# Performance work log

Measured on AMD Instinct MI355X. Metric: run time of the kernel, lower is better.

## Reference

```python
import jax, jax.numpy as jnp
import numpy as np

B, S, E, H, D = 384, 128, 512, 4, 128  # batch, seq(block), embed, heads, head_dim


def setup_inputs() -> dict:
    key = jax.random.key(0)
    ks = jax.random.split(key, 6)
    scale = 1.0 / np.sqrt(E)  # lecun_normal-ish fan-in scaling
    return {
        "x": jax.random.normal(ks[0], (B, S, E), dtype=jnp.float32),
        "Wq": jax.random.normal(ks[1], (E, E), dtype=jnp.float32) * scale,
        "bq": jnp.zeros((E,), dtype=jnp.float32),
        "Wk": jax.random.normal(ks[2], (E, E), dtype=jnp.float32) * scale,
        "bk": jnp.zeros((E,), dtype=jnp.float32),
        "Wv": jax.random.normal(ks[3], (E, E), dtype=jnp.float32) * scale,
        "bv": jnp.zeros((E,), dtype=jnp.float32),
        "Wo": jax.random.normal(ks[4], (E, E), dtype=jnp.float32) * scale,
        "bo": jnp.zeros((E,), dtype=jnp.float32),
    }


def reference(x, Wq, bq, Wk, bk, Wv, bv, Wo, bo):
    # Projections, then split heads: [B,S,E] -> [B,S,H,D]
    q = (x @ Wq + bq).reshape(B, S, H, D)
    k = (x @ Wk + bk).reshape(B, S, H, D)
    v = (x @ Wv + bv).reshape(B, S, H, D)
    # NOTE: original applies no 1/sqrt(D) scaling and no mask.
    scores = jnp.einsum("BSHD,BTHD->BHST", q, k)  # [B,H,S,T]
    weights = jax.nn.softmax(scores, axis=-1)
    out = jnp.einsum("BHST,BTHD->BSHD", weights, v).reshape(B, S, E)
    return out @ Wo + bo
```

## Files before the change

kernel.cpp:

```cpp
#include <hip/hip_runtime.h>
#include <hip/hip_bf16.h>
#include <cstdint>


#define EMB 512

typedef __attribute__((ext_vector_type(4))) float    f32x4;
typedef __attribute__((ext_vector_type(8))) _Float16 f16x8;

#define MFMA16(a, b, c) __builtin_amdgcn_mfma_f32_16x16x32_f16((a), (b), (c), 0, 0, 0)

__device__ __forceinline__ int swz128(int row, int col) {
    return row * 128 + (col ^ (((row >> 2) & 3) << 4));
}
__device__ __forceinline__ int swz64(int row, int col) {
    return row * 64 + (col ^ (((row >> 2) & 3) << 4));
}

__device__ __forceinline__ void gld_lds16(const _Float16* g, _Float16* l) {
    __builtin_amdgcn_global_load_lds(
        (const __attribute__((address_space(1))) void*)g,
        (__attribute__((address_space(3))) void*)l, 16, 0, 0);
}

__device__ __forceinline__ void stage64(_Float16* lds, const _Float16* gbase,
                                        int grow0, int k0, int wave, int lane) {
#pragma unroll
    for (int i = 0; i < 4; ++i) {
        int idx = wave * 256 + i * 64 + lane;
        int n   = idx >> 3;
        int kb  = (idx & 7) ^ (((n >> 2) & 3) << 1);
        gld_lds16(gbase + (grow0 + n) * EMB + k0 + kb * 8,
                  lds + wave * 2048 + i * 512);
    }
}

#define ZACC(A)                                   \
    _Pragma("unroll") for (int _i = 0; _i < 2; ++_i) \
    _Pragma("unroll") for (int _j = 0; _j < 8; ++_j) \
        A[_i][_j] = (f32x4){0.f, 0.f, 0.f, 0.f};

__global__ void k_prep(const float* __restrict__ x, _Float16* __restrict__ xh,
                       const float* __restrict__ Wq, const float* __restrict__ Wk,
                       const float* __restrict__ Wv, const float* __restrict__ Wo,
                       _Float16* __restrict__ Wqkvt, _Float16* __restrict__ Wot) {
    __shared__ float t[32][33];
    const int g = blockIdx.x, tid = threadIdx.x;
    if (g < 12288) {
        long i = ((long)g * 256 + tid) * 8;
        f32x4 a = *(const f32x4*)(x + i);
        f32x4 b = *(const f32x4*)(x + i + 4);
        f16x8 o;
        o[0] = (_Float16)a[0]; o[1] = (_Float16)a[1];
        o[2] = (_Float16)a[2]; o[3] = (_Float16)a[3];
        o[4] = (_Float16)b[0]; o[5] = (_Float16)b[1];
        o[6] = (_Float16)b[2]; o[7] = (_Float16)b[3];
        *(f16x8*)(xh + i) = o;
        return;
    }
    const int tb = g - 12288;
    const int z = tb >> 8, t2 = tb & 255;
    const float* W = (z == 0) ? Wq : (z == 1) ? Wk : (z == 2) ? Wv : Wo;
    _Float16* Wt = (z < 3) ? (Wqkvt + (long)z * 512 * EMB) : Wot;
    const int tx = tid & 31, ty = tid >> 5;
    const int k0 = (t2 & 15) * 32, n0 = (t2 >> 4) * 32;
#pragma unroll
    for (int i = 0; i < 4; ++i)
        t[ty + i * 8][tx] = W[(k0 + ty + i * 8) * EMB + n0 + tx];
    __syncthreads();
#pragma unroll
    for (int i = 0; i < 4; ++i)
        Wt[(n0 + ty + i * 8) * EMB + k0 + tx] = (_Float16)t[tx][ty + i * 8];
}

__global__ __launch_bounds__(256, 4)
void k_qkv(const _Float16* __restrict__ xh, const _Float16* __restrict__ Wqkvt,
           const float* __restrict__ bq, const float* __restrict__ bk,
           const float* __restrict__ bv,
           _Float16* __restrict__ qb, _Float16* __restrict__ kb,
           _Float16* __restrict__ vtb) {
    __shared__ _Float16 S[2][128 * 64];
    _Float16* SA = S[0];
    _Float16* SB = S[1];
    const int tid = threadIdx.x, wave = tid >> 6, lane = tid & 63;
    const int l15 = lane & 15, quad = lane >> 4;
    const int g = blockIdx.x;
    const int xcd = g & 7, r = g >> 3;
    const int bb = xcd * 48 + r / 12, j = r % 12;
    const int m0 = bb * 128;
    const bool vswap = (j >= 8);
    const _Float16* As = vswap ? SB : SA;
    const _Float16* Bs = vswap ? SA : SB;
    f32x4 acc[2][8];
    ZACC(acc);
    for (int k0 = 0; k0 < EMB; k0 += 64) {
        stage64(SA, xh, m0, k0, wave, lane);
        stage64(SB, Wqkvt, j * 128, k0, wave, lane);
        __syncthreads();
#pragma unroll
        for (int ktl = 0; ktl < 2; ++ktl) {
            int cb = ktl * 32 + quad * 8;
            f16x8 a0 = *(const f16x8*)&As[swz64(wave * 32 + l15, cb)];
            f16x8 a1 = *(const f16x8*)&As[swz64(wave * 32 + 16 + l15, cb)];
#pragma unroll
            for (int nt = 0; nt < 8; ++nt) {
                f16x8 bbf = *(const f16x8*)&Bs[swz64(nt * 16 + l15, cb)];
                acc[0][nt] = MFMA16(a0, bbf, acc[0][nt]);
                acc[1][nt] = MFMA16(a1, bbf, acc[1][nt]);
            }
        }
        __syncthreads();
    }
    _Float16* SC = &S[0][0];
    if (!vswap) {
        const float* bias = (j < 4) ? bq : bk;
        const int nc0 = (j & 3) * 128;
#pragma unroll
        for (int nt = 0; nt < 8; ++nt) {
            int col = nt * 16 + l15;
            float bz = bias[nc0 + col];
#pragma unroll
            for (int mt = 0; mt < 2; ++mt)
#pragma unroll
                for (int rr = 0; rr < 4; ++rr) {
                    int row = wave * 32 + mt * 16 + quad * 4 + rr;
                    SC[swz128(row, col)] = (_Float16)(acc[mt][nt][rr] + bz);
                }
        }
        __syncthreads();
        _Float16* dst = (j < 4) ? qb : kb;
#pragma unroll
        for (int i = 0; i < 8; ++i) {
            int idx = i * 256 + tid;
            int row = idx >> 4, col = (idx & 15) * 8;
            f16x8 v = *(const f16x8*)&SC[row * 128 + (col ^ (((row >> 2) & 3) << 4))];
            *(f16x8*)(dst + (long)(m0 + row) * EMB + nc0 + col) = v;
        }
    } else {
        const int hv = j - 8;
#pragma unroll
        for (int mt = 0; mt < 2; ++mt)
#pragma unroll
            for (int rr = 0; rr < 4; ++rr) {
                int row = wave * 32 + mt * 16 + quad * 4 + rr;
                float bz = bv[hv * 128 + row];
#pragma unroll
                for (int nt = 0; nt < 8; ++nt) {
                    int col = nt * 16 + l15;
                    SC[swz128(row, col)] = (_Float16)(acc[mt][nt][rr] + bz);
                }
            }
        __syncthreads();
        _Float16* dst = vtb + (long)(bb * 4 + hv) * 128 * 128;
#pragma unroll
        for (int i = 0; i < 8; ++i) {
            int idx = i * 256 + tid;
            int row = idx >> 4, col = (idx & 15) * 8;
            f16x8 v = *(const f16x8*)&SC[row * 128 + (col ^ (((row >> 2) & 3) << 4))];
            *(f16x8*)(dst + row * 128 + col) = v;
        }
    }
}

__global__ __launch_bounds__(512, 4)
void k_core(const _Float16* __restrict__ qb, const _Float16* __restrict__ kb,
            const _Float16* __restrict__ vtb, _Float16* __restrict__ attn) {
    __shared__ _Float16 SK[128 * 128];
    __shared__ _Float16 SV[128 * 128];
    const int tid = threadIdx.x, wave = tid >> 6, lane = tid & 63;
    const int l15 = lane & 15, quad = lane >> 4;
    const int g = blockIdx.x;
    const int xcd = g & 7, r = g >> 3;
    const int b = xcd * 48 + (r >> 2), h = r & 3;
    const int sRow0 = b * 128, wRow0 = h * 128;
    const _Float16* vt = vtb + (long)(b * 4 + h) * 128 * 128;

    f16x8 qf[4];
#pragma unroll
    for (int kt = 0; kt < 4; ++kt)
        qf[kt] = *(const f16x8*)(qb + (long)(sRow0 + wave * 16 + l15) * EMB +
                                 wRow0 + kt * 32 + quad * 8);
    __builtin_amdgcn_sched_barrier(0);
#pragma unroll
    for (int i = 0; i < 4; ++i) {
        int seg = i * 8 + wave;
        int idx = seg * 64 + lane;
        int n   = idx >> 4;
        int kbk = (idx & 15) ^ (((n >> 2) & 3) << 1);
        gld_lds16(kb + (long)(sRow0 + n) * EMB + wRow0 + kbk * 8, SK + seg * 512);
    }
    __builtin_amdgcn_sched_barrier(0);
#pragma unroll
    for (int i = 0; i < 4; ++i) {
        int seg = i * 8 + wave;
        int idx = seg * 64 + lane;
        int n   = idx >> 4;
        int kbk = (idx & 15) ^ (((n >> 2) & 3) << 1);
        gld_lds16(vt + n * 128 + kbk * 8, SV + seg * 512);
    }
    asm volatile("s_waitcnt vmcnt(4)" ::: "memory");
    __builtin_amdgcn_sched_barrier(0);
    __builtin_amdgcn_s_barrier();

    f32x4 acc[8];
#pragma unroll
    for (int nt = 0; nt < 8; ++nt) acc[nt] = (f32x4){0.f, 0.f, 0.f, 0.f};

    __builtin_amdgcn_s_setprio(1);
#pragma unroll
    for (int kt = 0; kt < 4; ++kt) {
        int ca = kt * 32 + quad * 8;
#pragma unroll
        for (int nt = 0; nt < 8; ++nt) {
            f16x8 kf = *(const f16x8*)&SK[swz128(nt * 16 + l15, ca)];
            acc[nt] = MFMA16(qf[kt], kf, acc[nt]);
        }
    }
    __builtin_amdgcn_s_setprio(0);
#pragma unroll
    for (int rr = 0; rr < 4; ++rr) {
        float mx = acc[0][rr];
#pragma unroll
        for (int nt = 1; nt < 8; ++nt) mx = fmaxf(mx, acc[nt][rr]);
        mx = fmaxf(mx, __shfl_xor(mx, 1));
        mx = fmaxf(mx, __shfl_xor(mx, 2));
        mx = fmaxf(mx, __shfl_xor(mx, 4));
        mx = fmaxf(mx, __shfl_xor(mx, 8));
        float sm = 0.f;
#pragma unroll
        for (int nt = 0; nt < 8; ++nt) {
            float e = __expf(acc[nt][rr] - mx);
            acc[nt][rr] = e;
            sm += e;
        }
        sm += __shfl_xor(sm, 1);
        sm += __shfl_xor(sm, 2);
        sm += __shfl_xor(sm, 4);
        sm += __shfl_xor(sm, 8);
        float inv = 1.0f / sm;
#pragma unroll
        for (int nt = 0; nt < 8; ++nt) acc[nt][rr] *= inv;
    }
    __syncthreads();

#pragma unroll
    for (int nt = 0; nt < 8; ++nt) {
        int col = nt * 16 + l15;
#pragma unroll
        for (int rr = 0; rr < 4; ++rr)
            SK[swz128(wave * 16 + quad * 4 + rr, col)] = (_Float16)acc[nt][rr];
    }
    __syncthreads();

#pragma unroll
    for (int nt = 0; nt < 8; ++nt) acc[nt] = (f32x4){0.f, 0.f, 0.f, 0.f};
    __builtin_amdgcn_s_setprio(1);
#pragma unroll
    for (int kt = 0; kt < 4; ++kt) {
        int ca = kt * 32 + quad * 8;
        f16x8 p0 = *(const f16x8*)&SK[swz128(wave * 16 + l15, ca)];
#pragma unroll
        for (int nt = 0; nt < 8; ++nt) {
            f16x8 vf = *(const f16x8*)&SV[swz128(nt * 16 + l15, ca)];
            acc[nt] = MFMA16(p0, vf, acc[nt]);
        }
    }
    __builtin_amdgcn_s_setprio(0);
    __syncthreads();

#pragma unroll
    for (int nt = 0; nt < 8; ++nt) {
        int col = nt * 16 + l15;
#pragma unroll
        for (int rr = 0; rr < 4; ++rr)
            SV[swz128(wave * 16 + quad * 4 + rr, col)] = (_Float16)acc[nt][rr];
    }
    __syncthreads();
#pragma unroll
    for (int i = 0; i < 4; ++i) {
        int idx = i * 512 + tid;
        int row = idx >> 4, col = (idx & 15) * 8;
        f16x8 v = *(const f16x8*)&SV[row * 128 + (col ^ (((row >> 2) & 3) << 4))];
        *(f16x8*)(attn + (long)(sRow0 + row) * EMB + wRow0 + col) = v;
    }
}

__global__ __launch_bounds__(256, 4)
void k_out(const _Float16* __restrict__ attn, const _Float16* __restrict__ Wot,
           const float* __restrict__ bo, float* __restrict__ out) {
    __shared__ _Float16 SH[16384];
    _Float16* SA = SH;
    _Float16* SB = SH + 4096;
    const int tid = threadIdx.x, wave = tid >> 6, lane = tid & 63;
    const int l15 = lane & 15, quad = lane >> 4;
    const int g = blockIdx.x;
    const int xcd = g & 7, r = g >> 3;
    const int m0 = (xcd * 96 + (r >> 2)) * 64, n0 = (r & 3) * 128;
    f32x4 acc[8];
#pragma unroll
    for (int nt = 0; nt < 8; ++nt) acc[nt] = (f32x4){0.f, 0.f, 0.f, 0.f};
    for (int k0 = 0; k0 < EMB; k0 += 64) {
#pragma unroll
        for (int i = 0; i < 2; ++i) {
            int seg = i * 4 + wave;
            int idx = seg * 64 + lane;
            int n = idx >> 3, kbk = (idx & 7) ^ (((n >> 2) & 3) << 1);
            gld_lds16(attn + (long)(m0 + n) * EMB + k0 + kbk * 8, SA + seg * 512);
        }
#pragma unroll
        for (int i = 0; i < 4; ++i) {
            int seg = i * 4 + wave;
            int idx = seg * 64 + lane;
            int n = idx >> 3, kbk = (idx & 7) ^ (((n >> 2) & 3) << 1);
            gld_lds16(Wot + (long)(n0 + n) * EMB + k0 + kbk * 8, SB + seg * 512);
        }
        __syncthreads();
#pragma unroll
        for (int ktl = 0; ktl < 2; ++ktl) {
            int cb = ktl * 32 + quad * 8;
            f16x8 a0 = *(const f16x8*)&SA[swz64(wave * 16 + l15, cb)];
#pragma unroll
            for (int nt = 0; nt < 8; ++nt) {
                f16x8 bb = *(const f16x8*)&SB[swz64(nt * 16 + l15, cb)];
                acc[nt] = MFMA16(a0, bb, acc[nt]);
            }
        }
        __syncthreads();
    }
    float* SF = (float*)SH;
#pragma unroll
    for (int nt = 0; nt < 8; ++nt) {
        int col = nt * 16 + l15;
        float bz = bo[n0 + col];
#pragma unroll
        for (int rr = 0; rr < 4; ++rr) {
            int row = wave * 16 + quad * 4 + rr;
            SF[row * 128 + (col ^ (((row >> 2) & 1) << 4))] = acc[nt][rr] + bz;
        }
    }
    __syncthreads();
#pragma unroll
    for (int i = 0; i < 8; ++i) {
        int idx = i * 256 + tid;
        int row = idx >> 5, c4 = (idx & 31) * 4;
        f32x4 v = *(const f32x4*)&SF[row * 128 + (c4 ^ (((row >> 2) & 1) << 4))];
        *(f32x4*)(out + (long)(m0 + row) * EMB + n0 + c4) = v;
    }
}

extern "C" void kernel_launch(void* const* d_in, const int* in_sizes, int n_in,
                              void* d_out, int out_size, void* d_ws, size_t ws_size,
                              hipStream_t stream) {
    const float* x  = (const float*)d_in[0];
    const float* Wq = (const float*)d_in[1];
    const float* bq = (const float*)d_in[2];
    const float* Wk = (const float*)d_in[3];
    const float* bk = (const float*)d_in[4];
    const float* Wv = (const float*)d_in[5];
    const float* bv = (const float*)d_in[6];
    const float* Wo = (const float*)d_in[7];
    const float* bo = (const float*)d_in[8];
    float* out = (float*)d_out;

    char* w = (char*)d_ws;
    _Float16* xh    = (_Float16*)(w);
    _Float16* attn  = xh;
    _Float16* Wqkvt = (_Float16*)(w + 50331648);
    _Float16* Wot   = (_Float16*)(w + 51904512);
    _Float16* qb    = (_Float16*)(w + 52428800);
    _Float16* kb    = (_Float16*)(w + 102760448);
    _Float16* vtb   = (_Float16*)(w + 153092096);

    k_prep<<<13312, 256, 0, stream>>>(x, xh, Wq, Wk, Wv, Wo, Wqkvt, Wot);
    k_qkv<<<4608, 256, 0, stream>>>(xh, Wqkvt, bq, bk, bv, qb, kb, vtb);
    k_core<<<1536, 512, 0, stream>>>(qb, kb, vtb, attn);
    k_out<<<3072, 256, 0, stream>>>(attn, Wot, bo, out);
}
```

Measured before the change: 365.1 us.

## Enlarge output-projection tile to 128 rows and drop a block barrier in attention

Result: no change. 362.6 us (-0.7%).

```diff
diff --git a/kernel.cpp b/kernel.cpp
--- a/kernel.cpp
+++ b/kernel.cpp
@@ -250,7 +250,8 @@
         for (int rr = 0; rr < 4; ++rr)
             SK[swz128(wave * 16 + quad * 4 + rr, col)] = (_Float16)acc[nt][rr];
     }
-    __syncthreads();
+    asm volatile("s_waitcnt lgkmcnt(0)" ::: "memory");
+    __builtin_amdgcn_sched_barrier(0);
 
 #pragma unroll
     for (int nt = 0; nt < 8; ++nt) acc[nt] = (f32x4){0.f, 0.f, 0.f, 0.f};
@@ -288,63 +289,59 @@
 __global__ __launch_bounds__(256, 4)
 void k_out(const _Float16* __restrict__ attn, const _Float16* __restrict__ Wot,
            const float* __restrict__ bo, float* __restrict__ out) {
-    __shared__ _Float16 SH[16384];
-    _Float16* SA = SH;
-    _Float16* SB = SH + 4096;
+    __shared__ _Float16 S[2][128 * 64];
+    _Float16* SA = S[0];
+    _Float16* SB = S[1];
     const int tid = threadIdx.x, wave = tid >> 6, lane = tid & 63;
     const int l15 = lane & 15, quad = lane >> 4;
     const int g = blockIdx.x;
     const int xcd = g & 7, r = g >> 3;
-    const int m0 = (xcd * 96 + (r >> 2)) * 64, n0 = (r & 3) * 128;
-    f32x4 acc[8];
-#pragma unroll
-    for (int nt = 0; nt < 8; ++nt) acc[nt] = (f32x4){0.f, 0.f, 0.f, 0.f};
+    const int m0 = (xcd * 48 + (r >> 2)) * 128, n0 = (r & 3) * 128;
+    f32x4 acc[2][8];
+    ZACC(acc);
     for (int k0 = 0; k0 < EMB; k0 += 64) {
-#pragma unroll
-        for (int i = 0; i < 2; ++i) {
-            int seg = i * 4 + wave;
-            int idx = seg * 64 + lane;
-            int n = idx >> 3, kbk = (idx & 7) ^ (((n >> 2) & 3) << 1);
-            gld_lds16(attn + (long)(m0 + n) * EMB + k0 + kbk * 8, SA + seg * 512);
-        }
-#pragma unroll
-        for (int i = 0; i < 4; ++i) {
-            int seg = i * 4 + wave;
-            int idx = seg * 64 + lane;
-            int n = idx >> 3, kbk = (idx & 7) ^ (((n >> 2) & 3) << 1);
-            gld_lds16(Wot + (long)(n0 + n) * EMB + k0 + kbk * 8, SB + seg * 512);
-        }
+        stage64(SA, attn, m0, k0, wave, lane);
+        stage64(SB, Wot, n0, k0, wave, lane);
         __syncthreads();
 #pragma unroll
         for (int ktl = 0; ktl < 2; ++ktl) {
             int cb = ktl * 32 + quad * 8;
-            f16x8 a0 = *(const f16x8*)&SA[swz64(wave * 16 + l15, cb)];
+            f16x8 a0 = *(const f16x8*)&SA[swz64(wave * 32 + l15, cb)];
+            f16x8 a1 = *(const f16x8*)&SA[swz64(wave * 32 + 16 + l15, cb)];
 #pragma unroll
             for (int nt = 0; nt < 8; ++nt) {
-                f16x8 bb = *(const f16x8*)&SB[swz64(nt * 16 + l15, cb)];
-                acc[nt] = MFMA16(a0, bb, acc[nt]);
+                f16x8 bbf = *(const f16x8*)&SB[swz64(nt * 16 + l15, cb)];
+                acc[0][nt] = MFMA16(a0, bbf, acc[0][nt]);
+                acc[1][nt] = MFMA16(a1, bbf, acc[1][nt]);
             }
         }
         __syncthreads();
     }
-    float* SF = (float*)SH;
-#pragma unroll
-    for (int nt = 0; nt < 8; ++nt) {
-        int col = nt * 16 + l15;
-        float bz = bo[n0 + col];
-#pragma unroll
-        for (int rr = 0; rr < 4; ++rr) {
-            int row = wave * 16 + quad * 4 + rr;
-            SF[row * 128 + (col ^ (((row >> 2) & 1) << 4))] = acc[nt][rr] + bz;
-        }
-    }
-    __syncthreads();
-#pragma unroll
-    for (int i = 0; i < 8; ++i) {
-        int idx = i * 256 + tid;
-        int row = idx >> 5, c4 = (idx & 31) * 4;
-        f32x4 v = *(const f32x4*)&SF[row * 128 + (c4 ^ (((row >> 2) & 1) << 4))];
-        *(f32x4*)(out + (long)(m0 + row) * EMB + n0 + c4) = v;
+    float* SF = (float*)&S[0][0];
+    float bz[8];
+#pragma unroll
+    for (int nt = 0; nt < 8; ++nt) bz[nt] = bo[n0 + nt * 16 + l15];
+#pragma unroll
+    for (int mt = 0; mt < 2; ++mt) {
+#pragma unroll
+        for (int nt = 0; nt < 8; ++nt) {
+            int col = nt * 16 + l15;
+#pragma unroll
+            for (int rr = 0; rr < 4; ++rr) {
+                int lr = wave * 16 + quad * 4 + rr;
+                SF[lr * 128 + (col ^ (((lr >> 2) & 1) << 4))] = acc[mt][nt][rr] + bz[nt];
+            }
+        }
+        __syncthreads();
+#pragma unroll
+        for (int i = 0; i < 8; ++i) {
+            int idx = i * 256 + tid;
+            int lr = idx >> 5, c4 = (idx & 31) * 4;
+            f32x4 v = *(const f32x4*)&SF[lr * 128 + (c4 ^ (((lr >> 2) & 1) << 4))];
+            int grow = (lr >> 4) * 32 + mt * 16 + (lr & 15);
+            *(f32x4*)(out + (long)(m0 + grow) * EMB + n0 + c4) = v;
+        }
+        __syncthreads();
     }
 }
 
@@ -374,5 +371,5 @@
     k_prep<<<13312, 256, 0, stream>>>(x, xh, Wq, Wk, Wv, Wo, Wqkvt, Wot);
     k_qkv<<<4608, 256, 0, stream>>>(xh, Wqkvt, bq, bk, bv, qb, kb, vtb);
     k_core<<<1536, 512, 0, stream>>>(qb, kb, vtb, attn);
-    k_out<<<3072, 256, 0, stream>>>(attn, Wot, bo, out);
-}
+    k_out<<<1536, 256, 0, stream>>>(attn, Wot, bo, out);
+}
```
